# Kernel tuning notes

Hardware: AMD Instinct MI355X
Metric: run time of the kernel (lower is better)

## Reference

```python
import jax, jax.numpy as jnp
import numpy as np

DIM = 512
HEADS = 8
DHEAD = 64
WIN = 128
QK_SCALE = 8.0
LN_EPS = 1e-5


def setup_inputs() -> dict:
    key = jax.random.key(0)
    ks = jax.random.split(key, 5)
    B, N = 8, 4096
    x = jax.random.normal(ks[0], (B, N, DIM), jnp.float32)
    w_qkv = jax.random.normal(ks[1], (3 * HEADS * DHEAD, DIM), jnp.float32) * 0.02
    w_out = jax.random.normal(ks[2], (DIM, HEADS * DHEAD), jnp.float32) * 0.02
    b_out = jnp.zeros((DIM,), jnp.float32)
    w_ff1 = jax.random.normal(ks[3], (4 * DIM, DIM), jnp.float32) * 0.02
    w_ff2 = jax.random.normal(ks[4], (DIM, 4 * DIM), jnp.float32) * 0.02
    return {
        'x': x, 'w_qkv': w_qkv,
        'q_scale': jnp.ones((DHEAD,), jnp.float32),
        'k_scale': jnp.ones((DHEAD,), jnp.float32),
        'w_out': w_out, 'b_out': b_out,
        'ln1_g': jnp.ones((DIM,), jnp.float32), 'ln1_b': jnp.zeros((DIM,), jnp.float32),
        'ff_ln_g': jnp.ones((DIM,), jnp.float32), 'ff_ln_b': jnp.zeros((DIM,), jnp.float32),
        'w_ff1': w_ff1, 'w_ff2': w_ff2,
    }


def _ln(x, g, b):
    m = jnp.mean(x, axis=-1, keepdims=True)
    v = jnp.mean((x - m) ** 2, axis=-1, keepdims=True)
    return (x - m) * jax.lax.rsqrt(v + LN_EPS) * g + b


def _l2norm(t):
    return t / jnp.clip(jnp.linalg.norm(t, axis=-1, keepdims=True), 1e-12)


def _rotary(t, pos):
    # t: (B, H, N, DHEAD); standard (non-xpos) rotary, half-split style
    inv_freq = 1.0 / (10000.0 ** (jnp.arange(0, DHEAD, 2, dtype=jnp.float32) / DHEAD))
    freqs = pos[:, None] * inv_freq                      # (N, DHEAD/2)
    emb = jnp.concatenate([freqs, freqs], axis=-1)       # (N, DHEAD)
    cos, sin = jnp.cos(emb), jnp.sin(emb)
    t1, t2 = t[..., : DHEAD // 2], t[..., DHEAD // 2:]
    rot = jnp.concatenate([-t2, t1], axis=-1)
    return t * cos + rot * sin


def reference(x, w_qkv, q_scale, k_scale, w_out, b_out, ln1_g, ln1_b,
              ff_ln_g, ff_ln_b, w_ff1, w_ff2):
    B, N, D = x.shape
    nw = N // WIN

    # ---- LocalMHA (prenorm, qk-rmsnorm, sliding window, causal) ----
    h = _ln(x, ln1_g, ln1_b)
    qkv = h @ w_qkv.T                                    # (B, N, 3*H*DHEAD)
    q, k, v = jnp.split(qkv, 3, axis=-1)

    def to_heads(t):
        return t.reshape(B, N, HEADS, DHEAD).transpose(0, 2, 1, 3)  # (B,H,N,d)

    q, k, v = to_heads(q), to_heads(k), to_heads(v)
    q = _l2norm(q) * q_scale
    k = _l2norm(k) * k_scale
    pos = jnp.arange(N, dtype=jnp.float32)
    q = _rotary(q, pos)
    k = _rotary(k, pos)

    # bucket into windows; keys/values look back one window
    bq = q.reshape(B, HEADS, nw, WIN, DHEAD)
    bk = k.reshape(B, HEADS, nw, WIN, DHEAD)
    bv = v.reshape(B, HEADS, nw, WIN, DHEAD)

    def look_back(t):
        prev = jnp.concatenate([jnp.zeros_like(t[:, :, :1]), t[:, :, :-1]], axis=2)
        return jnp.concatenate([prev, t], axis=3)

    kk, vv = look_back(bk), look_back(bv)

    qpos = jnp.arange(N, dtype=jnp.int32).reshape(nw, WIN)
    kprev = jnp.concatenate([jnp.full((1, WIN), -1, jnp.int32), qpos[:-1]], axis=0)
    kpos = jnp.concatenate([kprev, qpos], axis=1)
    mask = (qpos[:, :, None] >= kpos[:, None, :]) & (kpos[:, None, :] >= 0)

    sim = jnp.einsum('bhnid,bhnjd->bhnij', bq, kk) * QK_SCALE
    sim = jnp.where(mask, sim, -1e9)
    attn = jax.nn.softmax(sim, axis=-1)
    out = jnp.einsum('bhnij,bhnjd->bhnid', attn, vv)
    out = out.reshape(B, HEADS, N, DHEAD).transpose(0, 2, 1, 3).reshape(B, N, HEADS * DHEAD)
    x = x + out @ w_out.T + b_out

    # ---- FeedForward: LN -> Linear(4D, no bias) -> GELU -> Linear(D, no bias) ----
    hf = _ln(x, ff_ln_g, ff_ln_b)
    ff = jax.nn.gelu(hf @ w_ff1.T, approximate=False) @ w_ff2.T
    return x + ff
```

## Files before the change

kernel.cpp:

```cpp
#include <hip/hip_runtime.h>
#include <cstdint>
#include <cstddef>

typedef __bf16 bf16;
typedef __bf16 bf16x8 __attribute__((ext_vector_type(8)));
typedef float f32x4 __attribute__((ext_vector_type(4)));

#define DEV static __device__ __forceinline__

constexpr int BATCH = 8;
constexpr int SEQ = 4096;
constexpr int DIM = 512;
constexpr int HEADS = 8;
constexpr int DH = 64;
constexpr int WIN = 128;
constexpr int NW = SEQ / WIN;
constexpr int TOK = BATCH * SEQ;
constexpr float EPS = 1e-5f;

constexpr size_t R_EL   = (size_t)TOK * DIM;
constexpr size_t C_QKV  = 0;
constexpr size_t C_WOUT = 786432;
constexpr size_t C_WF1  = 1048576;
constexpr size_t C_WF2  = 2097152;
constexpr size_t C_SM   = 3145728;
constexpr size_t P_EL   = 3148416;

DEV void gload_lds16(const void* g, void* l) {
  __builtin_amdgcn_global_load_lds((__attribute__((address_space(1))) void*)g,
                                   (__attribute__((address_space(3))) void*)l,
                                   16, 0, 0);
}

DEV f32x4 mfma16(bf16x8 a, bf16x8 b, f32x4 c) {
  return __builtin_amdgcn_mfma_f32_16x16x32_bf16(a, b, c, 0, 0, 0);
}

DEV float fast_gelu(float v) {
  const float z = fabsf(v) * 0.7071067811865476f;
  const float t = __builtin_amdgcn_rcpf(1.0f + 0.3275911f * z);
  const float p = t * (0.254829592f +
                  t * (-0.284496736f +
                  t * (1.421413741f +
                  t * (-1.453152027f +
                  t * 1.061405429f))));
  const float e = __expf(-z * z);
  const float erfa = 1.0f - p * e;
  const float cdf = 0.5f + copysignf(0.5f * erfa, v);
  return v * cdf;
}

struct SrcPtrs { const void* p[12]; };

DEV void copy8(const void* src, long si, bf16* dst, bool f32) {
  if (f32) {
    const float4* s = (const float4*)((const float*)src + si);
    float4 a = s[0], b = s[1];
    bf16x8 o;
    o[0] = (bf16)a.x; o[1] = (bf16)a.y; o[2] = (bf16)a.z; o[3] = (bf16)a.w;
    o[4] = (bf16)b.x; o[5] = (bf16)b.y; o[6] = (bf16)b.z; o[7] = (bf16)b.w;
    *(bf16x8*)dst = o;
  } else {
    *(bf16x8*)dst = *(const bf16x8*)((const bf16*)src + si);
  }
}

__global__ __launch_bounds__(256) void ingest_kernel(SrcPtrs sp, bf16* cano) {
  const bool f32 = (((const unsigned short*)sp.p[2])[0] == 0);
  const long e = (long)threadIdx.x * 8;
  int b = blockIdx.x;
  if (b < 384)  { long o = (long)b * 2048 + e; copy8(sp.p[1], o, cano + C_QKV + o, f32); return; }
  b -= 384;
  if (b < 128)  { long o = (long)b * 2048 + e; copy8(sp.p[4], o, cano + C_WOUT + o, f32); return; }
  b -= 128;
  if (b < 512)  { long o = (long)b * 2048 + e; copy8(sp.p[10], o, cano + C_WF1 + o, f32); return; }
  b -= 512;
  if (b < 512)  { long o = (long)b * 2048 + e; copy8(sp.p[11], o, cano + C_WF2 + o, f32); return; }
  b -= 512;
  const long o = (long)b * 2048 + e;
  if (o >= 2688) return;
  const void* src; long si;
  if      (o < 64)   { src = sp.p[2]; si = o; }
  else if (o < 128)  { src = sp.p[3]; si = o - 64; }
  else if (o < 640)  { src = sp.p[5]; si = o - 128; }
  else if (o < 1152) { src = sp.p[6]; si = o - 640; }
  else if (o < 1664) { src = sp.p[7]; si = o - 1152; }
  else if (o < 2176) { src = sp.p[8]; si = o - 1664; }
  else               { src = sp.p[9]; si = o - 2176; }
  copy8(src, si, cano + C_SM + o, f32);
}

__global__ __launch_bounds__(256) void ln_kernel(const void* __restrict__ in,
                                                 const bf16* __restrict__ gg,
                                                 const bf16* __restrict__ bb,
                                                 bf16* __restrict__ out,
                                                 const unsigned short* __restrict__ probe,
                                                 int raw) {
  const int wave = threadIdx.x >> 6, lane = threadIdx.x & 63;
  const int row = blockIdx.x * 4 + wave;
  const size_t base = (size_t)row * DIM + lane * 8;
  float f[8];
  if (raw && probe[0] == 0) {
    const float4* p = (const float4*)((const float*)in + base);
    float4 a = p[0], bq = p[1];
    f[0] = a.x; f[1] = a.y; f[2] = a.z; f[3] = a.w;
    f[4] = bq.x; f[5] = bq.y; f[6] = bq.z; f[7] = bq.w;
  } else {
    bf16x8 v = *(const bf16x8*)((const bf16*)in + base);
#pragma unroll
    for (int i = 0; i < 8; ++i) f[i] = (float)v[i];
  }
  float s = 0.f, sq = 0.f;
#pragma unroll
  for (int i = 0; i < 8; ++i) { s += f[i]; sq += f[i] * f[i]; }
#pragma unroll
  for (int m = 32; m; m >>= 1) { s += __shfl_xor(s, m); sq += __shfl_xor(sq, m); }
  const float mean = s * (1.0f / DIM);
  const float var = fmaxf(sq * (1.0f / DIM) - mean * mean, 0.0f);
  const float rs = rsqrtf(var + EPS);
  bf16x8 gv = *(const bf16x8*)(gg + lane * 8);
  bf16x8 bv = *(const bf16x8*)(bb + lane * 8);
  bf16x8 o;
#pragma unroll
  for (int i = 0; i < 8; ++i) o[i] = (bf16)((f[i] - mean) * rs * (float)gv[i] + (float)bv[i]);
  *(bf16x8*)((bf16*)out + base) = o;
}

template <int MODE>
__global__ __launch_bounds__(512) void gemm_bt(const bf16* __restrict__ A,
                                               const bf16* __restrict__ Bw,
                                               bf16* __restrict__ O0, bf16* __restrict__ O1,
                                               bf16* __restrict__ O2,
                                               float* __restrict__ Of,
                                               const void* __restrict__ Xraw,
                                               const bf16* __restrict__ Xb,
                                               const bf16* __restrict__ bias,
                                               const unsigned short* __restrict__ probe,
                                               int K, int bstride, int ostride, int gx) {
  extern __shared__ __align__(16) bf16 smem[];
  const int tid = threadIdx.x;
  const int wid = tid >> 6, lane = tid & 63;
  const int l15 = lane & 15, quad = lane >> 4;
  const int id = blockIdx.x;
  const int per = gx * 8;
  const int tM = ((id / per) * 8 + (id & 7)) * 256;
  const int tN = ((id % per) >> 3) * 128;
  const int wM = (wid >> 1) * 64, wN = (wid & 1) * 64;
  const int kq = (quad ^ ((l15 >> 1) & 3)) * 8;
  f32x4 acc[4][4];
  const f32x4 z = {0.f, 0.f, 0.f, 0.f};
#pragma unroll
  for (int i = 0; i < 4; ++i)
#pragma unroll
    for (int j = 0; j < 4; ++j) acc[i][j] = z;

  const int cA0 = tid,       rA0 = cA0 >> 2, sA0 = (((cA0 & 3) ^ ((cA0 >> 3) & 3)) * 8);
  const int cA1 = tid + 512, rA1 = cA1 >> 2, sA1 = (((cA1 & 3) ^ ((cA1 >> 3) & 3)) * 8);
  const int cB0 = tid,       rB0 = cB0 >> 2, sB0 = sA0;

  auto stage = [&](int t, int p) {
    const int k0 = t * 32;
    bf16* dA = smem + p * 12288;
    bf16* dB = dA + 8192;
    gload_lds16(A  + (size_t)(tM + rA0) * K       + k0 + sA0, &dA[cA0 * 8]);
    gload_lds16(A  + (size_t)(tM + rA1) * K       + k0 + sA1, &dA[cA1 * 8]);
    gload_lds16(Bw + (size_t)(tN + rB0) * bstride + k0 + sB0, &dB[cB0 * 8]);
  };

  const int nt = K >> 5;
  stage(0, 0);
  stage(1, 1);
  __builtin_amdgcn_sched_barrier(0);
  asm volatile("s_waitcnt vmcnt(3)" ::: "memory");
  __builtin_amdgcn_s_barrier();
  __builtin_amdgcn_sched_barrier(0);

  int cur = 0;
  for (int t = 0; t < nt; ++t) {
    if (t + 2 < nt) {
      int nx = cur + 2; if (nx >= 3) nx -= 3;
      stage(t + 2, nx);
    }
    const bf16* As = smem + cur * 12288;
    const bf16* Bs = As + 8192;
    bf16x8 aF[4], bF[4];
#pragma unroll
    for (int i = 0; i < 4; ++i) aF[i] = *(const bf16x8*)&As[(wM + i * 16 + l15) * 32 + kq];
#pragma unroll
    for (int j = 0; j < 4; ++j) bF[j] = *(const bf16x8*)&Bs[(wN + j * 16 + l15) * 32 + kq];
#pragma unroll
    for (int i = 0; i < 4; ++i)
#pragma unroll
      for (int j = 0; j < 4; ++j) acc[i][j] = mfma16(aF[i], bF[j], acc[i][j]);
    if (t < nt - 1) {
      __builtin_amdgcn_sched_barrier(0);
      if (t + 2 < nt) asm volatile("s_waitcnt vmcnt(3)" ::: "memory");
      else            asm volatile("s_waitcnt vmcnt(0)" ::: "memory");
      __builtin_amdgcn_s_barrier();
      __builtin_amdgcn_sched_barrier(0);
    }
    ++cur; if (cur == 3) cur = 0;
  }
  const int q0 = nt % 3;
  int q1 = q0 + 1; if (q1 == 3) q1 = 0;
  bf16* eb = smem + q0 * 12288;

  if constexpr (MODE == 0) {
    bf16* ob = eb + wid * 1152;
    const int colbase = tN + wN;
    const int which = colbase >> 9;
    const int head = (colbase >> 6) & 7;
    bf16* dst = which == 0 ? O0 : (which == 1 ? O1 : O2);
    const int ch = lane & 7;
    float scv[8], invf[8];
    if (which < 2) {
      const bf16* sc = which ? bias : Xb;
      bf16x8 s8 = *(const bf16x8*)(sc + ch * 8);
#pragma unroll
      for (int u = 0; u < 8; ++u) {
        scv[u] = (float)s8[u] * (which == 0 ? 8.0f : 1.0f);
        invf[u] = exp2f(-(float)((ch & 3) * 8 + u) * (13.287712379549449f / 32.0f));
      }
    }
#pragma unroll
    for (int i = 0; i < 4; ++i) {
#pragma unroll
      for (int j = 0; j < 4; ++j)
#pragma unroll
        for (int r = 0; r < 4; ++r)
          ob[(quad * 4 + r) * 72 + j * 16 + l15] = (bf16)acc[i][j][r];
#pragma unroll
      for (int t = 0; t < 2; ++t) {
        const int rr = t * 8 + (lane >> 3);
        const int rowg = tM + wM + i * 16 + rr;
        bf16x8 ov = *(const bf16x8*)&ob[rr * 72 + ch * 8];
        float f[8];
#pragma unroll
        for (int u = 0; u < 8; ++u) f[u] = (float)ov[u];
        if (which < 2) {
          float ss = 0.f;
#pragma unroll
          for (int u = 0; u < 8; ++u) ss += f[u] * f[u];
          ss += __shfl_xor(ss, 1); ss += __shfl_xor(ss, 2); ss += __shfl_xor(ss, 4);
          const float rs = 1.0f / fmaxf(sqrtf(ss), 1e-12f);
#pragma unroll
          for (int u = 0; u < 8; ++u) f[u] *= rs * scv[u];
          float pf[8];
#pragma unroll
          for (int u = 0; u < 8; ++u) pf[u] = __shfl_xor(f[u], 4);
          const float pos = (float)(rowg & (SEQ - 1));
#pragma unroll
          for (int u = 0; u < 8; ++u) {
            float sn, cs;
            __sincosf(pos * invf[u], &sn, &cs);
            const float rot = (ch < 4) ? -pf[u] : pf[u];
            f[u] = f[u] * cs + rot * sn;
          }
        }
        bf16x8 o8;
#pragma unroll
        for (int u = 0; u < 8; ++u) o8[u] = (bf16)f[u];
        const int bb = rowg >> 12, n = rowg & (SEQ - 1);
        *(bf16x8*)(dst + ((size_t)(bb * HEADS + head) * SEQ + n) * DH + ch * 8) = o8;
      }
    }
    return;
  }

  if constexpr (MODE == 1 || MODE == 2) {
    bf16* ob = eb + wid * 1152;
    const int ch = lane & 7;
    bf16x8 bias8;
    bool xf32 = false;
    if constexpr (MODE == 1) {
      bias8 = *(const bf16x8*)(bias + tN + wN + ch * 8);
      xf32 = (probe[0] == 0);
    }
#pragma unroll
    for (int i = 0; i < 4; ++i) {
#pragma unroll
      for (int j = 0; j < 4; ++j)
#pragma unroll
        for (int r = 0; r < 4; ++r)
          ob[(quad * 4 + r) * 72 + j * 16 + l15] = (bf16)acc[i][j][r];
#pragma unroll
      for (int t = 0; t < 2; ++t) {
        const int rr = t * 8 + (lane >> 3);
        const int rowg = tM + wM + i * 16 + rr;
        bf16x8 ov = *(const bf16x8*)&ob[rr * 72 + ch * 8];
        bf16x8 o8;
        if constexpr (MODE == 1) {
          const size_t idx = (size_t)rowg * DIM + tN + wN + ch * 8;
          float xr[8];
          if (xf32) {
            const float4* xp = (const float4*)((const float*)Xraw + idx);
            float4 a = xp[0], bq = xp[1];
            xr[0] = a.x; xr[1] = a.y; xr[2] = a.z; xr[3] = a.w;
            xr[4] = bq.x; xr[5] = bq.y; xr[6] = bq.z; xr[7] = bq.w;
          } else {
            bf16x8 xv = *(const bf16x8*)((const bf16*)Xraw + idx);
#pragma unroll
            for (int u = 0; u < 8; ++u) xr[u] = (float)xv[u];
          }
#pragma unroll
          for (int u = 0; u < 8; ++u) o8[u] = (bf16)((float)ov[u] + xr[u] + (float)bias8[u]);
          *(bf16x8*)(O0 + idx) = o8;
        } else {
#pragma unroll
          for (int u = 0; u < 8; ++u) o8[u] = (bf16)fast_gelu((float)ov[u]);
          *(bf16x8*)(O0 + (size_t)rowg * ostride + tN + wN + ch * 8) = o8;
        }
      }
    }
    return;
  }

  if constexpr (MODE == 3 || MODE == 4) {
    float* obf = (wid < 6)
        ? (float*)(smem + q0 * 12288) + wid * 1024
        : (float*)(smem + q1 * 12288) + (wid - 6) * 1024;
    const int ch = lane & 7;
#pragma unroll
    for (int i = 0; i < 4; ++i) {
#pragma unroll
      for (int j = 0; j < 4; ++j)
#pragma unroll
        for (int r = 0; r < 4; ++r)
          obf[(quad * 4 + r) * 64 + j * 16 + l15] = acc[i][j][r];
#pragma unroll
      for (int t = 0; t < 2; ++t) {
        const int rr = t * 8 + (lane >> 3);
        const int rowg = tM + wM + i * 16 + rr;
        const size_t idx = (size_t)rowg * DIM + tN + wN + ch * 8;
        const float4* rp = (const float4*)&obf[rr * 64 + ch * 8];
        float4 a = rp[0], b = rp[1];
        float f[8] = {a.x, a.y, a.z, a.w, b.x, b.y, b.z, b.w};
        if constexpr (MODE == 3) {
          bf16x8 xv = *(const bf16x8*)(Xb + idx);
#pragma unroll
          for (int u = 0; u < 8; ++u) f[u] += (float)xv[u];
        } else {
          const float4* op = (const float4*)(Of + idx);
          float4 oa = op[0], ob4 = op[1];
          f[0] += oa.x; f[1] += oa.y; f[2] += oa.z; f[3] += oa.w;
          f[4] += ob4.x; f[5] += ob4.y; f[6] += ob4.z; f[7] += ob4.w;
        }
        float4 o0 = {f[0], f[1], f[2], f[3]}, o1 = {f[4], f[5], f[6], f[7]};
        ((float4*)(Of + idx))[0] = o0;
        ((float4*)(Of + idx))[1] = o1;
      }
    }
    return;
  }
}

__global__ __launch_bounds__(256, 3) void attn_kernel(const bf16* __restrict__ q,
                                                      const bf16* __restrict__ k,
                                                      const bf16* __restrict__ v,
                                                      bf16* __restrict__ ao) {
  __shared__ __align__(16) bf16 kv[256 * 72];
  __shared__ __align__(16) bf16 pbuf[4][16 * 136];
  const int w = blockIdx.x, h = blockIdx.y, b = blockIdx.z;
  const int tid = threadIdx.x;
  const int wv = tid >> 6, lane = tid & 63;
  const int l15 = lane & 15, quad = lane >> 4;
  const size_t bh = (size_t)b * HEADS + h;
  const bf16* qb = q + bh * SEQ * DH;
  const bf16* kb = k + bh * SEQ * DH;
  const bf16* vb = v + bh * SEQ * DH;
  const int t0 = (w - 1) * WIN;

#pragma unroll
  for (int it = 0; it < 8; ++it) {
    const int c = it * 256 + tid;
    const int tok = c >> 3, ch = c & 7;
    int gt = t0 + tok; gt = gt < 0 ? 0 : gt;
    *(bf16x8*)&kv[tok * 72 + ch * 8] = *(const bf16x8*)(kb + (size_t)gt * DH + ch * 8);
  }
  bf16x8 aQ[2][2];
#pragma unroll
  for (int qt = 0; qt < 2; ++qt) {
    const int qtok = w * WIN + wv * 32 + qt * 16 + l15;
#pragma unroll
    for (int ks = 0; ks < 2; ++ks)
      aQ[qt][ks] = *(const bf16x8*)(qb + (size_t)qtok * DH + ks * 32 + quad * 8);
  }
  int gtv = t0 + tid; gtv = gtv < 0 ? 0 : gtv;
  bf16x8 vld[8];
#pragma unroll
  for (int dg = 0; dg < 8; ++dg)
    vld[dg] = *(const bf16x8*)(vb + (size_t)gtv * DH + dg * 8);
  __syncthreads();

  bf16x8 aP[2][8];
#pragma unroll
  for (int qt = 0; qt < 2; ++qt) {
    f32x4 sreg[16];
#pragma unroll
    for (int nt = 0; nt < 16; ++nt) {
      f32x4 a = {0.f, 0.f, 0.f, 0.f};
#pragma unroll
      for (int ks = 0; ks < 2; ++ks) {
        bf16x8 bK = *(const bf16x8*)&kv[(nt * 16 + l15) * 72 + ks * 32 + quad * 8];
        a = mfma16(aQ[qt][ks], bK, a);
      }
      sreg[nt] = a;
    }
    const int qlb = wv * 32 + qt * 16 + quad * 4;
    float rinv[4];
#pragma unroll
    for (int r = 0; r < 4; ++r) {
      const int ql = qlb + r;
      float sum = 0.f;
#pragma unroll
      for (int nt = 0; nt < 16; ++nt) {
        const int j = nt * 16 + l15;
        const bool valid = (nt < 8) ? (w > 0) : (ql >= j - WIN);
        const float p = valid ? __expf(sreg[nt][r]) : 0.0f;
        sreg[nt][r] = p;
        sum += p;
      }
#pragma unroll
      for (int m = 8; m; m >>= 1) sum += __shfl_xor(sum, m);
      rinv[r] = 1.0f / sum;
    }
#pragma unroll
    for (int half = 0; half < 2; ++half) {
#pragma unroll
      for (int ntw = 0; ntw < 8; ++ntw)
#pragma unroll
        for (int r = 0; r < 4; ++r)
          pbuf[wv][(quad * 4 + r) * 136 + ntw * 16 + l15] =
              (bf16)(sreg[half * 8 + ntw][r] * rinv[r]);
#pragma unroll
      for (int kk = 0; kk < 4; ++kk)
        aP[qt][half * 4 + kk] = *(const bf16x8*)&pbuf[wv][l15 * 136 + kk * 32 + quad * 8];
    }
  }
  __syncthreads();

#pragma unroll
  for (int dg = 0; dg < 8; ++dg)
#pragma unroll
    for (int i = 0; i < 8; ++i)
      kv[(dg * 8 + i) * 264 + tid] = vld[dg][i];
  __syncthreads();

#pragma unroll
  for (int qt = 0; qt < 2; ++qt) {
#pragma unroll
    for (int dt = 0; dt < 4; ++dt) {
      f32x4 o = {0.f, 0.f, 0.f, 0.f};
#pragma unroll
      for (int ks2 = 0; ks2 < 8; ++ks2) {
        bf16x8 bV = *(const bf16x8*)&kv[(dt * 16 + l15) * 264 + ks2 * 32 + quad * 8];
        o = mfma16(aP[qt][ks2], bV, o);
      }
#pragma unroll
      for (int r = 0; r < 4; ++r)
        pbuf[wv][(quad * 4 + r) * 136 + dt * 16 + l15] = (bf16)o[r];
    }
#pragma unroll
    for (int t = 0; t < 2; ++t) {
      const int rr = t * 8 + (lane >> 3), ch = lane & 7;
      bf16x8 ov = *(const bf16x8*)&pbuf[wv][rr * 136 + ch * 8];
      const int tok = w * WIN + wv * 32 + qt * 16 + rr;
      *(bf16x8*)(ao + ((size_t)b * SEQ + tok) * DIM + h * DH + ch * 8) = ov;
    }
  }
}

extern "C" void kernel_launch(void* const* d_in, const int* in_sizes, int n_in,
                              void* d_out, int out_size, void* d_ws, size_t ws_size,
                              hipStream_t stream) {
  (void)in_sizes; (void)n_in; (void)out_size;
  float* out = (float*)d_out;
  bf16* cano = (bf16*)d_ws;
  const unsigned short* probe = (const unsigned short*)d_in[2];

  SrcPtrs sp;
  for (int i = 0; i < 12; ++i) sp.p[i] = d_in[i];

  bf16* slot0 = cano + P_EL;
  bf16* slot1 = cano + P_EL + R_EL;
  bf16* slot2 = cano + P_EL + 2 * R_EL;
  bf16* slot3 = cano + P_EL + 3 * R_EL;

  const bf16* qsc  = cano + C_SM + 0;
  const bf16* ksc  = cano + C_SM + 64;
  const bf16* bout = cano + C_SM + 128;
  const bf16* l1g  = cano + C_SM + 640;
  const bf16* l1b  = cano + C_SM + 1152;
  const bf16* lfg  = cano + C_SM + 1664;
  const bf16* lfb  = cano + C_SM + 2176;

  constexpr int LDSB = 3 * 12288 * 2;
  static bool attr_done = false;
  if (!attr_done) {
    hipFuncSetAttribute((const void*)gemm_bt<0>, hipFuncAttributeMaxDynamicSharedMemorySize, LDSB);
    hipFuncSetAttribute((const void*)gemm_bt<1>, hipFuncAttributeMaxDynamicSharedMemorySize, LDSB);
    hipFuncSetAttribute((const void*)gemm_bt<2>, hipFuncAttributeMaxDynamicSharedMemorySize, LDSB);
    hipFuncSetAttribute((const void*)gemm_bt<3>, hipFuncAttributeMaxDynamicSharedMemorySize, LDSB);
    hipFuncSetAttribute((const void*)gemm_bt<4>, hipFuncAttributeMaxDynamicSharedMemorySize, LDSB);
    attr_done = true;
  }

  ingest_kernel<<<1538, 256, 0, stream>>>(sp, cano);
  ln_kernel<<<TOK / 4, 256, 0, stream>>>(d_in[0], l1g, l1b, slot0, probe, 1);
  gemm_bt<0><<<16 * 96, 512, LDSB, stream>>>(slot0, cano + C_QKV, slot1, slot2, slot3,
                                             nullptr, nullptr, qsc, ksc, probe,
                                             DIM, DIM, 0, 12);
  attn_kernel<<<dim3(NW, HEADS, BATCH), 256, 0, stream>>>(slot1, slot2, slot3, slot0);
  gemm_bt<1><<<16 * 32, 512, LDSB, stream>>>(slot0, cano + C_WOUT, slot1, nullptr, nullptr,
                                             nullptr, d_in[0], nullptr, bout, probe,
                                             DIM, DIM, 0, 4);
  ln_kernel<<<TOK / 4, 256, 0, stream>>>(slot1, lfg, lfb, slot0, probe, 0);

  const bool big = ws_size >= (size_t)(P_EL + 6 * R_EL) * 2;
  if (big) {
    bf16* f1 = slot2;
    gemm_bt<2><<<16 * 128, 512, LDSB, stream>>>(slot0, cano + C_WF1, f1, nullptr, nullptr,
                                                nullptr, nullptr, nullptr, nullptr, probe,
                                                DIM, DIM, 2048, 16);
    gemm_bt<3><<<16 * 32, 512, LDSB, stream>>>(f1, cano + C_WF2, nullptr, nullptr, nullptr,
                                               out, nullptr, slot1, nullptr, probe,
                                               2048, 2048, 0, 4);
  } else {
    bf16* f1h = slot2;
    for (int half = 0; half < 2; ++half) {
      const bf16* w1h = cano + C_WF1 + (size_t)half * 1024 * DIM;
      const bf16* w2h = cano + C_WF2 + (size_t)half * 1024;
      gemm_bt<2><<<16 * 64, 512, LDSB, stream>>>(slot0, w1h, f1h, nullptr, nullptr,
                                                 nullptr, nullptr, nullptr, nullptr, probe,
                                                 DIM, DIM, 1024, 8);
      if (half == 0)
        gemm_bt<3><<<16 * 32, 512, LDSB, stream>>>(f1h, w2h, nullptr, nullptr, nullptr,
                                                   out, nullptr, slot1, nullptr, probe,
                                                   1024, 2048, 0, 4);
      else
        gemm_bt<4><<<16 * 32, 512, LDSB, stream>>>(f1h, w2h, nullptr, nullptr, nullptr,
                                                   out, nullptr, nullptr, nullptr, probe,
                                                   1024, 2048, 0, 4);
    }
  }
}
```

Measured before the change: 479.1 us.

## Fuse FFN up-projection, GELU and down-projection into one kernel

Replaces the two FFN GEMM launches with a single kernel. Each block owns 128 token rows, computes 128-wide chunks of the hidden activation with GELU into LDS, and immediately accumulates the down-projection in registers. This removes the global round trip of the 4x-wide intermediate activation and extra launches. In exchange, one block of 256 gives limited parallelism, and the W2 fragments are read directly from global memory without LDS staging.

```diff
diff --git a/kernel.cpp b/kernel.cpp
--- a/kernel.cpp
+++ b/kernel.cpp
@@ -202,7 +202,6 @@
     ++cur; if (cur == 3) cur = 0;
   }
   const int q0 = nt % 3;
-  int q1 = q0 + 1; if (q1 == 3) q1 = 0;
   bf16* eb = smem + q0 * 12288;
 
   if constexpr (MODE == 0) {
@@ -267,15 +266,11 @@
     return;
   }
 
-  if constexpr (MODE == 1 || MODE == 2) {
+  if constexpr (MODE == 1) {
     bf16* ob = eb + wid * 1152;
     const int ch = lane & 7;
-    bf16x8 bias8;
-    bool xf32 = false;
-    if constexpr (MODE == 1) {
-      bias8 = *(const bf16x8*)(bias + tN + wN + ch * 8);
-      xf32 = (probe[0] == 0);
-    }
+    bf16x8 bias8 = *(const bf16x8*)(bias + tN + wN + ch * 8);
+    const bool xf32 = (probe[0] == 0);
 #pragma unroll
     for (int i = 0; i < 4; ++i) {
 #pragma unroll
@@ -289,69 +284,172 @@
         const int rowg = tM + wM + i * 16 + rr;
         bf16x8 ov = *(const bf16x8*)&ob[rr * 72 + ch * 8];
         bf16x8 o8;
-        if constexpr (MODE == 1) {
-          const size_t idx = (size_t)rowg * DIM + tN + wN + ch * 8;
-          float xr[8];
-          if (xf32) {
-            const float4* xp = (const float4*)((const float*)Xraw + idx);
-            float4 a = xp[0], bq = xp[1];
-            xr[0] = a.x; xr[1] = a.y; xr[2] = a.z; xr[3] = a.w;
-            xr[4] = bq.x; xr[5] = bq.y; xr[6] = bq.z; xr[7] = bq.w;
-          } else {
-            bf16x8 xv = *(const bf16x8*)((const bf16*)Xraw + idx);
-#pragma unroll
-            for (int u = 0; u < 8; ++u) xr[u] = (float)xv[u];
-          }
-#pragma unroll
-          for (int u = 0; u < 8; ++u) o8[u] = (bf16)((float)ov[u] + xr[u] + (float)bias8[u]);
-          *(bf16x8*)(O0 + idx) = o8;
+        const size_t idx = (size_t)rowg * DIM + tN + wN + ch * 8;
+        float xr[8];
+        if (xf32) {
+          const float4* xp = (const float4*)((const float*)Xraw + idx);
+          float4 a = xp[0], bq = xp[1];
+          xr[0] = a.x; xr[1] = a.y; xr[2] = a.z; xr[3] = a.w;
+          xr[4] = bq.x; xr[5] = bq.y; xr[6] = bq.z; xr[7] = bq.w;
         } else {
-#pragma unroll
-          for (int u = 0; u < 8; ++u) o8[u] = (bf16)fast_gelu((float)ov[u]);
-          *(bf16x8*)(O0 + (size_t)rowg * ostride + tN + wN + ch * 8) = o8;
+          bf16x8 xv = *(const bf16x8*)((const bf16*)Xraw + idx);
+#pragma unroll
+          for (int u = 0; u < 8; ++u) xr[u] = (float)xv[u];
         }
+#pragma unroll
+        for (int u = 0; u < 8; ++u) o8[u] = (bf16)((float)ov[u] + xr[u] + (float)bias8[u]);
+        *(bf16x8*)(O0 + idx) = o8;
       }
     }
     return;
   }
-
-  if constexpr (MODE == 3 || MODE == 4) {
-    float* obf = (wid < 6)
-        ? (float*)(smem + q0 * 12288) + wid * 1024
-        : (float*)(smem + q1 * 12288) + (wid - 6) * 1024;
-    const int ch = lane & 7;
-#pragma unroll
-    for (int i = 0; i < 4; ++i) {
-#pragma unroll
-      for (int j = 0; j < 4; ++j)
+}
+
+__global__ __launch_bounds__(512, 2) void ffn_fused(const bf16* __restrict__ hf,
+                                                    const bf16* __restrict__ W1,
+                                                    const bf16* __restrict__ W2,
+                                                    const bf16* __restrict__ x2,
+                                                    float* __restrict__ out) {
+  extern __shared__ __align__(16) bf16 smem[];
+  const int tid = threadIdx.x;
+  const int wid = tid >> 6, lane = tid & 63;
+  const int l15 = lane & 15, quad = lane >> 4;
+  const int tM = blockIdx.x * 128;
+  const int wM  = (wid >> 2) * 64;
+  const int wN1 = (wid & 3) * 32;
+  const int wN2 = (wid & 3) * 128;
+  const int kq = (quad ^ ((l15 >> 1) & 3)) * 8;
+  bf16* f1c = smem + 24576;
+
+  const int srow = tid >> 2;
+  const int scol = ((tid & 3) ^ ((tid >> 3) & 3)) * 8;
+
+  auto stage1 = [&](int cc, int t, int p) {
+    const int k0 = t * 32;
+    bf16* dH = smem + p * 8192;
+    bf16* dW = dH + 4096;
+    gload_lds16(hf + (size_t)(tM + srow) * DIM + k0 + scol, &dH[tid * 8]);
+    gload_lds16(W1 + (size_t)(cc * 128 + srow) * DIM + k0 + scol, &dW[tid * 8]);
+  };
+
+  f32x4 acc2[4][8];
+  const f32x4 z = {0.f, 0.f, 0.f, 0.f};
+#pragma unroll
+  for (int i = 0; i < 4; ++i)
+#pragma unroll
+    for (int j = 0; j < 8; ++j) acc2[i][j] = z;
+
+  stage1(0, 0, 0);
+  stage1(0, 1, 1);
+  __builtin_amdgcn_sched_barrier(0);
+  asm volatile("s_waitcnt vmcnt(2)" ::: "memory");
+  __builtin_amdgcn_s_barrier();
+  __builtin_amdgcn_sched_barrier(0);
+
+  for (int c = 0; c < 16; ++c) {
+    f32x4 acc1[4][2];
+#pragma unroll
+    for (int i = 0; i < 4; ++i) { acc1[i][0] = z; acc1[i][1] = z; }
+    int cur = 0;
+    for (int t = 0; t < 16; ++t) {
+      if (t + 2 < 16) {
+        int nx = cur + 2; if (nx >= 3) nx -= 3;
+        stage1(c, t + 2, nx);
+      }
+      const bf16* Hs = smem + cur * 8192;
+      const bf16* Ws = Hs + 4096;
+      bf16x8 aF[4], bF[2];
+#pragma unroll
+      for (int i = 0; i < 4; ++i) aF[i] = *(const bf16x8*)&Hs[(wM + i * 16 + l15) * 32 + kq];
+#pragma unroll
+      for (int j = 0; j < 2; ++j) bF[j] = *(const bf16x8*)&Ws[(wN1 + j * 16 + l15) * 32 + kq];
+#pragma unroll
+      for (int i = 0; i < 4; ++i)
+#pragma unroll
+        for (int j = 0; j < 2; ++j) acc1[i][j] = mfma16(aF[i], bF[j], acc1[i][j]);
+      if (t < 15) {
+        __builtin_amdgcn_sched_barrier(0);
+        if (t + 2 < 16) asm volatile("s_waitcnt vmcnt(2)" ::: "memory");
+        else            asm volatile("s_waitcnt vmcnt(0)" ::: "memory");
+        __builtin_amdgcn_s_barrier();
+        __builtin_amdgcn_sched_barrier(0);
+      }
+      ++cur; if (cur == 3) cur = 0;
+    }
+    __builtin_amdgcn_sched_barrier(0);
+    __builtin_amdgcn_s_barrier();
+    __builtin_amdgcn_sched_barrier(0);
+#pragma unroll
+    for (int i = 0; i < 4; ++i)
+#pragma unroll
+      for (int j = 0; j < 2; ++j)
+#pragma unroll
+        for (int r = 0; r < 4; ++r) {
+          const int rowW = wM + i * 16 + quad * 4 + r;
+          const int colW = wN1 + j * 16 + l15;
+          f1c[rowW * 128 + ((((colW >> 3) ^ (rowW & 7))) << 3) + (colW & 7)] =
+              (bf16)fast_gelu(acc1[i][j][r]);
+        }
+    if (c < 15) { stage1(c + 1, 0, 0); stage1(c + 1, 1, 1); }
+    asm volatile("s_waitcnt lgkmcnt(0)" ::: "memory");
+    __builtin_amdgcn_sched_barrier(0);
+    __builtin_amdgcn_s_barrier();
+    __builtin_amdgcn_sched_barrier(0);
+    const bf16* w2c = W2 + c * 128;
+#pragma unroll
+    for (int kk = 0; kk < 4; ++kk) {
+      bf16x8 a2[4], b2[8];
+#pragma unroll
+      for (int i = 0; i < 4; ++i) {
+        const int row = wM + i * 16 + l15;
+        a2[i] = *(const bf16x8*)&f1c[row * 128 + (((kk * 4 + quad) ^ (l15 & 7)) << 3)];
+      }
+#pragma unroll
+      for (int j = 0; j < 8; ++j)
+        b2[j] = *(const bf16x8*)(w2c + (size_t)(wN2 + j * 16 + l15) * 2048 + kk * 32 + quad * 8);
+#pragma unroll
+      for (int i = 0; i < 4; ++i)
+#pragma unroll
+        for (int j = 0; j < 8; ++j) acc2[i][j] = mfma16(a2[i], b2[j], acc2[i][j]);
+    }
+    if (c < 15) {
+      __builtin_amdgcn_sched_barrier(0);
+      asm volatile("s_waitcnt vmcnt(2)" ::: "memory");
+      __builtin_amdgcn_s_barrier();
+      __builtin_amdgcn_sched_barrier(0);
+    }
+  }
+
+  __builtin_amdgcn_sched_barrier(0);
+  __builtin_amdgcn_s_barrier();
+  __builtin_amdgcn_sched_barrier(0);
+  float* obf = (float*)f1c + wid * 1024;
+  const int ch = lane & 7;
+#pragma unroll
+  for (int i = 0; i < 4; ++i)
+#pragma unroll
+    for (int jh = 0; jh < 2; ++jh) {
+#pragma unroll
+      for (int j2 = 0; j2 < 4; ++j2)
 #pragma unroll
         for (int r = 0; r < 4; ++r)
-          obf[(quad * 4 + r) * 64 + j * 16 + l15] = acc[i][j][r];
+          obf[(quad * 4 + r) * 64 + j2 * 16 + l15] = acc2[i][jh * 4 + j2][r];
 #pragma unroll
       for (int t = 0; t < 2; ++t) {
         const int rr = t * 8 + (lane >> 3);
         const int rowg = tM + wM + i * 16 + rr;
-        const size_t idx = (size_t)rowg * DIM + tN + wN + ch * 8;
+        const size_t idx = (size_t)rowg * DIM + wN2 + jh * 64 + ch * 8;
         const float4* rp = (const float4*)&obf[rr * 64 + ch * 8];
         float4 a = rp[0], b = rp[1];
         float f[8] = {a.x, a.y, a.z, a.w, b.x, b.y, b.z, b.w};
-        if constexpr (MODE == 3) {
-          bf16x8 xv = *(const bf16x8*)(Xb + idx);
-#pragma unroll
-          for (int u = 0; u < 8; ++u) f[u] += (float)xv[u];
-        } else {
-          const float4* op = (const float4*)(Of + idx);
-          float4 oa = op[0], ob4 = op[1];
-          f[0] += oa.x; f[1] += oa.y; f[2] += oa.z; f[3] += oa.w;
-          f[4] += ob4.x; f[5] += ob4.y; f[6] += ob4.z; f[7] += ob4.w;
-        }
+        bf16x8 xv = *(const bf16x8*)(x2 + idx);
+#pragma unroll
+        for (int u = 0; u < 8; ++u) f[u] += (float)xv[u];
         float4 o0 = {f[0], f[1], f[2], f[3]}, o1 = {f[4], f[5], f[6], f[7]};
-        ((float4*)(Of + idx))[0] = o0;
-        ((float4*)(Of + idx))[1] = o1;
-      }
-    }
-    return;
-  }
+        ((float4*)(out + idx))[0] = o0;
+        ((float4*)(out + idx))[1] = o1;
+      }
+    }
 }
 
 __global__ __launch_bounds__(256, 3) void attn_kernel(const bf16* __restrict__ q,
@@ -473,7 +571,7 @@
 extern "C" void kernel_launch(void* const* d_in, const int* in_sizes, int n_in,
                               void* d_out, int out_size, void* d_ws, size_t ws_size,
                               hipStream_t stream) {
-  (void)in_sizes; (void)n_in; (void)out_size;
+  (void)in_sizes; (void)n_in; (void)out_size; (void)ws_size;
   float* out = (float*)d_out;
   bf16* cano = (bf16*)d_ws;
   const unsigned short* probe = (const unsigned short*)d_in[2];
@@ -495,13 +593,12 @@
   const bf16* lfb  = cano + C_SM + 2176;
 
   constexpr int LDSB = 3 * 12288 * 2;
+  constexpr int LDSF = 81920;
   static bool attr_done = false;
   if (!attr_done) {
     hipFuncSetAttribute((const void*)gemm_bt<0>, hipFuncAttributeMaxDynamicSharedMemorySize, LDSB);
     hipFuncSetAttribute((const void*)gemm_bt<1>, hipFuncAttributeMaxDynamicSharedMemorySize, LDSB);
-    hipFuncSetAttribute((const void*)gemm_bt<2>, hipFuncAttributeMaxDynamicSharedMemorySize, LDSB);
-    hipFuncSetAttribute((const void*)gemm_bt<3>, hipFuncAttributeMaxDynamicSharedMemorySize, LDSB);
-    hipFuncSetAttribute((const void*)gemm_bt<4>, hipFuncAttributeMaxDynamicSharedMemorySize, LDSB);
+    hipFuncSetAttribute((const void*)ffn_fused, hipFuncAttributeMaxDynamicSharedMemorySize, LDSF);
     attr_done = true;
   }
 
@@ -515,32 +612,6 @@
                                              nullptr, d_in[0], nullptr, bout, probe,
                                              DIM, DIM, 0, 4);
   ln_kernel<<<TOK / 4, 256, 0, stream>>>(slot1, lfg, lfb, slot0, probe, 0);
-
-  const bool big = ws_size >= (size_t)(P_EL + 6 * R_EL) * 2;
-  if (big) {
-    bf16* f1 = slot2;
-    gemm_bt<2><<<16 * 128, 512, LDSB, stream>>>(slot0, cano + C_WF1, f1, nullptr, nullptr,
-                                                nullptr, nullptr, nullptr, nullptr, probe,
-                                                DIM, DIM, 2048, 16);
-    gemm_bt<3><<<16 * 32, 512, LDSB, stream>>>(f1, cano + C_WF2, nullptr, nullptr, nullptr,
-                                               out, nullptr, slot1, nullptr, probe,
-                                               2048, 2048, 0, 4);
-  } else {
-    bf16* f1h = slot2;
-    for (int half = 0; half < 2; ++half) {
-      const bf16* w1h = cano + C_WF1 + (size_t)half * 1024 * DIM;
-      const bf16* w2h = cano + C_WF2 + (size_t)half * 1024;
-      gemm_bt<2><<<16 * 64, 512, LDSB, stream>>>(slot0, w1h, f1h, nullptr, nullptr,
-                                                 nullptr, nullptr, nullptr, nullptr, probe,
-                                                 DIM, DIM, 1024, 8);
-      if (half == 0)
-        gemm_bt<3><<<16 * 32, 512, LDSB, stream>>>(f1h, w2h, nullptr, nullptr, nullptr,
-                                                   out, nullptr, slot1, nullptr, probe,
-                                                   1024, 2048, 0, 4);
-      else
-        gemm_bt<4><<<16 * 32, 512, LDSB, stream>>>(f1h, w2h, nullptr, nullptr, nullptr,
-                                                   out, nullptr, nullptr, nullptr, probe,
-                                                   1024, 2048, 0, 4);
-    }
-  }
-}
+  ffn_fused<<<TOK / 128, 512, LDSF, stream>>>(slot0, cano + C_WF1, cano + C_WF2,
+                                              slot1, out);
+}
```

After: 552.6 us. 15.3% more time.

## Use dedicated 256x256-tile GEMM kernel for feed-forward layers

Applied to the files above, without the earlier changes.

Adds a gemm_ff kernel with 256x256 output tiles (each wave computes 128x64 using 8x4 MFMA accumulators) for the two FFN GEMMs, replacing the smaller-tile generic gemm_bt path. Larger tiles raise arithmetic intensity and reduce redundant global loads of A and B for the FFN matmuls, which dominate FLOPs. In exchange, register pressure doubles for the accumulators, LDS use per block grows, and there are fewer blocks in the grid, which can hurt occupancy and tail balance.

```diff
diff --git a/kernel.cpp b/kernel.cpp
--- a/kernel.cpp
+++ b/kernel.cpp
@@ -202,7 +202,6 @@
     ++cur; if (cur == 3) cur = 0;
   }
   const int q0 = nt % 3;
-  int q1 = q0 + 1; if (q1 == 3) q1 = 0;
   bf16* eb = smem + q0 * 12288;
 
   if constexpr (MODE == 0) {
@@ -267,15 +266,11 @@
     return;
   }
 
-  if constexpr (MODE == 1 || MODE == 2) {
+  if constexpr (MODE == 1) {
     bf16* ob = eb + wid * 1152;
     const int ch = lane & 7;
-    bf16x8 bias8;
-    bool xf32 = false;
-    if constexpr (MODE == 1) {
-      bias8 = *(const bf16x8*)(bias + tN + wN + ch * 8);
-      xf32 = (probe[0] == 0);
-    }
+    bf16x8 bias8 = *(const bf16x8*)(bias + tN + wN + ch * 8);
+    const bool xf32 = (probe[0] == 0);
 #pragma unroll
     for (int i = 0; i < 4; ++i) {
 #pragma unroll
@@ -289,39 +284,129 @@
         const int rowg = tM + wM + i * 16 + rr;
         bf16x8 ov = *(const bf16x8*)&ob[rr * 72 + ch * 8];
         bf16x8 o8;
-        if constexpr (MODE == 1) {
-          const size_t idx = (size_t)rowg * DIM + tN + wN + ch * 8;
-          float xr[8];
-          if (xf32) {
-            const float4* xp = (const float4*)((const float*)Xraw + idx);
-            float4 a = xp[0], bq = xp[1];
-            xr[0] = a.x; xr[1] = a.y; xr[2] = a.z; xr[3] = a.w;
-            xr[4] = bq.x; xr[5] = bq.y; xr[6] = bq.z; xr[7] = bq.w;
-          } else {
-            bf16x8 xv = *(const bf16x8*)((const bf16*)Xraw + idx);
-#pragma unroll
-            for (int u = 0; u < 8; ++u) xr[u] = (float)xv[u];
-          }
-#pragma unroll
-          for (int u = 0; u < 8; ++u) o8[u] = (bf16)((float)ov[u] + xr[u] + (float)bias8[u]);
-          *(bf16x8*)(O0 + idx) = o8;
+        const size_t idx = (size_t)rowg * DIM + tN + wN + ch * 8;
+        float xr[8];
+        if (xf32) {
+          const float4* xp = (const float4*)((const float*)Xraw + idx);
+          float4 a = xp[0], bq = xp[1];
+          xr[0] = a.x; xr[1] = a.y; xr[2] = a.z; xr[3] = a.w;
+          xr[4] = bq.x; xr[5] = bq.y; xr[6] = bq.z; xr[7] = bq.w;
         } else {
-#pragma unroll
-          for (int u = 0; u < 8; ++u) o8[u] = (bf16)fast_gelu((float)ov[u]);
-          *(bf16x8*)(O0 + (size_t)rowg * ostride + tN + wN + ch * 8) = o8;
+          bf16x8 xv = *(const bf16x8*)((const bf16*)Xraw + idx);
+#pragma unroll
+          for (int u = 0; u < 8; ++u) xr[u] = (float)xv[u];
         }
+#pragma unroll
+        for (int u = 0; u < 8; ++u) o8[u] = (bf16)((float)ov[u] + xr[u] + (float)bias8[u]);
+        *(bf16x8*)(O0 + idx) = o8;
       }
     }
     return;
   }
+}
+
+template <int MODE>
+__global__ __launch_bounds__(512, 2) void gemm_ff(const bf16* __restrict__ A,
+                                                  const bf16* __restrict__ Bw,
+                                                  bf16* __restrict__ O0,
+                                                  float* __restrict__ Of,
+                                                  const bf16* __restrict__ Xb,
+                                                  int K, int bstride, int ostride, int gx) {
+  extern __shared__ __align__(16) bf16 smem[];
+  const int tid = threadIdx.x;
+  const int wid = tid >> 6, lane = tid & 63;
+  const int l15 = lane & 15, quad = lane >> 4;
+  const int id = blockIdx.x;
+  const int per = gx * 8;
+  const int tM = ((id / per) * 8 + (id & 7)) * 256;
+  const int tN = ((id % per) >> 3) * 256;
+  const int wm = (wid >> 2) * 128, wn = (wid & 3) * 64;
+  const int kq = (quad ^ ((l15 >> 1) & 3)) * 8;
+  f32x4 acc[8][4];
+  const f32x4 z = {0.f, 0.f, 0.f, 0.f};
+#pragma unroll
+  for (int i = 0; i < 8; ++i)
+#pragma unroll
+    for (int j = 0; j < 4; ++j) acc[i][j] = z;
+
+  const int c0 = tid,       r0 = c0 >> 2, s0 = (((c0 & 3) ^ ((c0 >> 3) & 3)) * 8);
+  const int c1 = tid + 512, r1 = c1 >> 2, s1 = (((c1 & 3) ^ ((c1 >> 3) & 3)) * 8);
+
+  auto stage = [&](int t, int p) {
+    const int k0 = t * 32;
+    bf16* dA = smem + p * 16384;
+    bf16* dB = dA + 8192;
+    gload_lds16(A  + (size_t)(tM + r0) * K       + k0 + s0, &dA[c0 * 8]);
+    gload_lds16(A  + (size_t)(tM + r1) * K       + k0 + s1, &dA[c1 * 8]);
+    gload_lds16(Bw + (size_t)(tN + r0) * bstride + k0 + s0, &dB[c0 * 8]);
+    gload_lds16(Bw + (size_t)(tN + r1) * bstride + k0 + s1, &dB[c1 * 8]);
+  };
+
+  const int nt = K >> 5;
+  stage(0, 0);
+  stage(1, 1);
+  __builtin_amdgcn_sched_barrier(0);
+  asm volatile("s_waitcnt vmcnt(4)" ::: "memory");
+  __builtin_amdgcn_s_barrier();
+  __builtin_amdgcn_sched_barrier(0);
+
+  int cur = 0;
+  for (int t = 0; t < nt; ++t) {
+    if (t + 2 < nt) {
+      int nx = cur + 2; if (nx >= 3) nx -= 3;
+      stage(t + 2, nx);
+    }
+    const bf16* As = smem + cur * 16384;
+    const bf16* Bs = As + 8192;
+    bf16x8 aF[8], bF[4];
+#pragma unroll
+    for (int i = 0; i < 8; ++i) aF[i] = *(const bf16x8*)&As[(wm + i * 16 + l15) * 32 + kq];
+#pragma unroll
+    for (int j = 0; j < 4; ++j) bF[j] = *(const bf16x8*)&Bs[(wn + j * 16 + l15) * 32 + kq];
+#pragma unroll
+    for (int i = 0; i < 8; ++i)
+#pragma unroll
+      for (int j = 0; j < 4; ++j) acc[i][j] = mfma16(aF[i], bF[j], acc[i][j]);
+    if (t < nt - 1) {
+      __builtin_amdgcn_sched_barrier(0);
+      if (t + 2 < nt) asm volatile("s_waitcnt vmcnt(4)" ::: "memory");
+      else            asm volatile("s_waitcnt vmcnt(0)" ::: "memory");
+      __builtin_amdgcn_s_barrier();
+      __builtin_amdgcn_sched_barrier(0);
+    }
+    ++cur; if (cur == 3) cur = 0;
+  }
+  const int q0 = nt % 3;
+  bf16* eb = smem + q0 * 16384;
+  const int ch = lane & 7;
+
+  if constexpr (MODE == 2) {
+    bf16* ob = eb + wid * 1152;
+#pragma unroll
+    for (int i = 0; i < 8; ++i) {
+#pragma unroll
+      for (int j = 0; j < 4; ++j)
+#pragma unroll
+        for (int r = 0; r < 4; ++r)
+          ob[(quad * 4 + r) * 72 + j * 16 + l15] = (bf16)acc[i][j][r];
+#pragma unroll
+      for (int t = 0; t < 2; ++t) {
+        const int rr = t * 8 + (lane >> 3);
+        const int rowg = tM + wm + i * 16 + rr;
+        bf16x8 ov = *(const bf16x8*)&ob[rr * 72 + ch * 8];
+        bf16x8 o8;
+#pragma unroll
+        for (int u = 0; u < 8; ++u) o8[u] = (bf16)fast_gelu((float)ov[u]);
+        *(bf16x8*)(O0 + (size_t)rowg * ostride + tN + wn + ch * 8) = o8;
+      }
+    }
+    return;
+  }
 
   if constexpr (MODE == 3 || MODE == 4) {
-    float* obf = (wid < 6)
-        ? (float*)(smem + q0 * 12288) + wid * 1024
-        : (float*)(smem + q1 * 12288) + (wid - 6) * 1024;
-    const int ch = lane & 7;
-#pragma unroll
-    for (int i = 0; i < 4; ++i) {
+    float* obf = (float*)eb + wid * 1024;
+#pragma unroll
+    for (int i = 0; i < 8; ++i) {
 #pragma unroll
       for (int j = 0; j < 4; ++j)
 #pragma unroll
@@ -330,8 +415,8 @@
 #pragma unroll
       for (int t = 0; t < 2; ++t) {
         const int rr = t * 8 + (lane >> 3);
-        const int rowg = tM + wM + i * 16 + rr;
-        const size_t idx = (size_t)rowg * DIM + tN + wN + ch * 8;
+        const int rowg = tM + wm + i * 16 + rr;
+        const size_t idx = (size_t)rowg * DIM + tN + wn + ch * 8;
         const float4* rp = (const float4*)&obf[rr * 64 + ch * 8];
         float4 a = rp[0], b = rp[1];
         float f[8] = {a.x, a.y, a.z, a.w, b.x, b.y, b.z, b.w};
@@ -495,13 +580,14 @@
   const bf16* lfb  = cano + C_SM + 2176;
 
   constexpr int LDSB = 3 * 12288 * 2;
+  constexpr int LDSF = 3 * 16384 * 2;
   static bool attr_done = false;
   if (!attr_done) {
     hipFuncSetAttribute((const void*)gemm_bt<0>, hipFuncAttributeMaxDynamicSharedMemorySize, LDSB);
     hipFuncSetAttribute((const void*)gemm_bt<1>, hipFuncAttributeMaxDynamicSharedMemorySize, LDSB);
-    hipFuncSetAttribute((const void*)gemm_bt<2>, hipFuncAttributeMaxDynamicSharedMemorySize, LDSB);
-    hipFuncSetAttribute((const void*)gemm_bt<3>, hipFuncAttributeMaxDynamicSharedMemorySize, LDSB);
-    hipFuncSetAttribute((const void*)gemm_bt<4>, hipFuncAttributeMaxDynamicSharedMemorySize, LDSB);
+    hipFuncSetAttribute((const void*)gemm_ff<2>, hipFuncAttributeMaxDynamicSharedMemorySize, LDSF);
+    hipFuncSetAttribute((const void*)gemm_ff<3>, hipFuncAttributeMaxDynamicSharedMemorySize, LDSF);
+    hipFuncSetAttribute((const void*)gemm_ff<4>, hipFuncAttributeMaxDynamicSharedMemorySize, LDSF);
     attr_done = true;
   }
 
@@ -519,28 +605,23 @@
   const bool big = ws_size >= (size_t)(P_EL + 6 * R_EL) * 2;
   if (big) {
     bf16* f1 = slot2;
-    gemm_bt<2><<<16 * 128, 512, LDSB, stream>>>(slot0, cano + C_WF1, f1, nullptr, nullptr,
-                                                nullptr, nullptr, nullptr, nullptr, probe,
-                                                DIM, DIM, 2048, 16);
-    gemm_bt<3><<<16 * 32, 512, LDSB, stream>>>(f1, cano + C_WF2, nullptr, nullptr, nullptr,
-                                               out, nullptr, slot1, nullptr, probe,
-                                               2048, 2048, 0, 4);
+    gemm_ff<2><<<16 * 64, 512, LDSF, stream>>>(slot0, cano + C_WF1, f1, nullptr, nullptr,
+                                               DIM, DIM, 2048, 8);
+    gemm_ff<3><<<16 * 16, 512, LDSF, stream>>>(f1, cano + C_WF2, nullptr, out, slot1,
+                                               2048, 2048, 0, 2);
   } else {
     bf16* f1h = slot2;
     for (int half = 0; half < 2; ++half) {
       const bf16* w1h = cano + C_WF1 + (size_t)half * 1024 * DIM;
       const bf16* w2h = cano + C_WF2 + (size_t)half * 1024;
-      gemm_bt<2><<<16 * 64, 512, LDSB, stream>>>(slot0, w1h, f1h, nullptr, nullptr,
-                                                 nullptr, nullptr, nullptr, nullptr, probe,
-                                                 DIM, DIM, 1024, 8);
+      gemm_ff<2><<<16 * 32, 512, LDSF, stream>>>(slot0, w1h, f1h, nullptr, nullptr,
+                                                 DIM, DIM, 1024, 4);
       if (half == 0)
-        gemm_bt<3><<<16 * 32, 512, LDSB, stream>>>(f1h, w2h, nullptr, nullptr, nullptr,
-                                                   out, nullptr, slot1, nullptr, probe,
-                                                   1024, 2048, 0, 4);
+        gemm_ff<3><<<16 * 16, 512, LDSF, stream>>>(f1h, w2h, nullptr, out, slot1,
+                                                   1024, 2048, 0, 2);
       else
-        gemm_bt<4><<<16 * 32, 512, LDSB, stream>>>(f1h, w2h, nullptr, nullptr, nullptr,
-                                                   out, nullptr, nullptr, nullptr, probe,
-                                                   1024, 2048, 0, 4);
-    }
-  }
-}
+        gemm_ff<4><<<16 * 16, 512, LDSF, stream>>>(f1h, w2h, nullptr, out, nullptr,
+                                                   1024, 2048, 0, 2);
+    }
+  }
+}
```

New measurement: 499.2 us. +4.2%, slower.
